# Performance work log

Hardware: AMD Instinct MI355X
Metric: run time of the kernel (lower is better)

The kernel has to match this reference:

```python
import jax, jax.numpy as jnp
import numpy as np

N_HEAD = 16
T0 = 1.0        # eta schedule reference time
C_LOG = 3.0     # fixed eta(t) = C_LOG * log(t / T0)  (mode='log', non-learnable default)
ETA_CLIP = 50.0 # eta clamped to [-ETA_CLIP, ETA_CLIP] before exponentiation


def setup_inputs() -> dict:
    key = jax.random.key(0)
    k0, k1, k2 = jax.random.split(key, 3)
    B, T, D = 2, 2048, 1024
    x = jax.random.normal(k0, (B, T, D), dtype=jnp.float32)
    ln_weight = jnp.ones((D,), dtype=jnp.float32)  # LayerNorm weight (bias=False per cfg)
    c_attn_w = jax.random.normal(k1, (3 * D, D), dtype=jnp.float32) * 0.02  # torch Linear weight [3D, D]
    c_proj_w = jax.random.normal(k2, (D, D), dtype=jnp.float32) * 0.02      # output proj [D, D]
    # theta_h = inv_softplus(1.0) so that step size h = softplus(theta_h) = 1.0
    theta_h = jnp.asarray(np.log(np.expm1(1.0)), dtype=jnp.float32)
    return {"x": x, "ln_weight": ln_weight, "c_attn_w": c_attn_w,
            "c_proj_w": c_proj_w, "theta_h": theta_h}


def _layer_norm(x, w, eps=1e-5):
    mu = jnp.mean(x, axis=-1, keepdims=True)
    var = jnp.var(x, axis=-1, keepdims=True)
    return (x - mu) * jax.lax.rsqrt(var + eps) * w


def reference(x, ln_weight, c_attn_w, c_proj_w, theta_h):
    B, T, D = x.shape
    H = N_HEAD
    hd = D // H

    y = _layer_norm(x, ln_weight)
    qkv = jnp.einsum('btd,ed->bte', y, c_attn_w)        # [B, T, 3D]
    q, k, v = jnp.split(qkv, 3, axis=-1)
    q = q.reshape(B, T, H, hd).transpose(0, 2, 1, 3)    # [B, H, T, hd]
    k = k.reshape(B, T, H, hd).transpose(0, 2, 1, 3)
    v = v.reshape(B, T, H, hd).transpose(0, 2, 1, 3)

    # time-dependent conformal/symplectic scaling: t_i = t0 + h*i, eta = c_log*log(t/t0)
    h = jax.nn.softplus(theta_h)
    t = T0 + h * jnp.arange(T, dtype=jnp.float32)
    eta = jnp.clip(C_LOG * jnp.log(t / T0), -ETA_CLIP, ETA_CLIP)  # [T]
    q = q * jnp.exp(eta)[None, None, :, None]    # query scaled by exp(+eta(t_i))
    k = k * jnp.exp(-eta)[None, None, :, None]   # key scaled by exp(-eta(t_j))

    att = jnp.einsum('bhqd,bhkd->bhqk', q, k) / jnp.sqrt(jnp.float32(hd))
    mask = jnp.tril(jnp.ones((T, T), dtype=bool))  # causal: keep j <= i
    att = jnp.where(mask[None, None], att, -jnp.inf)
    att = jax.nn.softmax(att, axis=-1)

    out = jnp.einsum('bhqk,bhkd->bhqd', att, v)
    out = out.transpose(0, 2, 1, 3).reshape(B, T, D)
    return jnp.einsum('btd,ed->bte', out, c_proj_w)
```

## Files before the change

kernel.cpp:

```cpp
#include <hip/hip_runtime.h>
#include <stdint.h>
#include <stddef.h>

typedef __attribute__((ext_vector_type(8))) short short8;
typedef __attribute__((ext_vector_type(4))) float float4v;

#define T_SEQ 2048
#define D_MODEL 1024
#define NH 16
#define HD 64

static __device__ __forceinline__ unsigned short f2bf(float f) {
  unsigned u = __builtin_bit_cast(unsigned, f);
  u += 0x7fffu + ((u >> 16) & 1u);
  return (unsigned short)(u >> 16);
}
static __device__ __forceinline__ float bf2f(unsigned short h) {
  unsigned u = ((unsigned)h) << 16;
  return __builtin_bit_cast(float, u);
}
static __device__ __forceinline__ float4v mfma16(short8 a, short8 b, float4v c) {
  return __builtin_amdgcn_mfma_f32_16x16x32_bf16(a, b, c, 0, 0, 0);
}
static __device__ __forceinline__ void split3(float f, unsigned short& h0,
                                              unsigned short& h1, unsigned short& h2) {
  h0 = f2bf(f);
  float r1 = f - bf2f(h0);
  h1 = f2bf(r1);
  float r2 = r1 - bf2f(h1);
  h2 = f2bf(r2);
}
static __device__ __forceinline__ void split2(float f, unsigned short& h0, unsigned short& h1) {
  h0 = f2bf(f);
  h1 = f2bf(f - bf2f(h0));
}

static __device__ __forceinline__ void stage16(const unsigned short* g, unsigned short* l) {
#if __has_builtin(__builtin_amdgcn_global_load_lds)
  __builtin_amdgcn_global_load_lds(
      (const __attribute__((address_space(1))) unsigned int*)g,
      (__attribute__((address_space(3))) unsigned int*)l, 16, 0, 0);
#else
  *(short8*)l = *(const short8*)g;
#endif
}

__global__ __launch_bounds__(256) void prep_kernel(
    const float* x, const float* wgt, const float* attn_w, const float* theta,
    unsigned short* y0, unsigned short* y1, unsigned short* y2,
    unsigned short* W0, unsigned short* W1, unsigned short* W2,
    float* E, float* Einv) {
  __shared__ float rs[4], rq[4];
  int bx = blockIdx.x;
  int tid = threadIdx.x;
  if (bx < 4096) {
    int row = bx;
    const float* xr = x + (size_t)row * D_MODEL;
    float v[4];
    float sum = 0.f, ssq = 0.f;
    for (int it = 0; it < 4; ++it) {
      float f = xr[tid + 256 * it];
      v[it] = f;
      sum += f; ssq += f * f;
    }
    for (int off = 32; off >= 1; off >>= 1) {
      sum += __shfl_xor(sum, off, 64);
      ssq += __shfl_xor(ssq, off, 64);
    }
    int w = tid >> 6;
    if ((tid & 63) == 0) { rs[w] = sum; rq[w] = ssq; }
    __syncthreads();
    sum = rs[0] + rs[1] + rs[2] + rs[3];
    ssq = rq[0] + rq[1] + rq[2] + rq[3];
    float mu = sum * (1.0f / D_MODEL);
    float var = ssq * (1.0f / D_MODEL) - mu * mu;
    float rstd = rsqrtf(var + 1e-5f);
    for (int it = 0; it < 4; ++it) {
      int d = tid + 256 * it;
      float y = (v[it] - mu) * rstd * wgt[d];
      unsigned short h0, h1, h2;
      split3(y, h0, h1, h2);
      size_t o = (size_t)row * D_MODEL + d;
      y0[o] = h0; y1[o] = h1; y2[o] = h2;
    }
  } else if (bx < 5632) {
    size_t base = ((size_t)(bx - 4096) * 256 + tid) * 8;
    int row = (int)(base >> 10);
    short8 a, b, c;
    for (int j = 0; j < 8; ++j) {
      unsigned short h0, h1, h2;
      split3(attn_w[base + j], h0, h1, h2);
      a[j] = (short)h0; b[j] = (short)h1; c[j] = (short)h2;
    }
    *(short8*)(W0 + base) = a;
    *(short8*)(W1 + base) = b;
    if (row < 2048) *(short8*)(W2 + base) = c;
  } else {
    int i = (bx - 5632) * 256 + tid;
    if (i < T_SEQ) {
      float th = theta[0];
      float h = log1pf(expf(th));
      float t = 1.0f + h * (float)i;
      float eta = 3.0f * logf(t);
      eta = fminf(fmaxf(eta, -50.0f), 50.0f);
      E[i] = expf(eta);
      Einv[i] = expf(-eta);
    }
  }
}

__global__ __launch_bounds__(256) void conv_pw(const float* src, unsigned short* P0,
                                               unsigned short* P1) {
  size_t base = ((size_t)blockIdx.x * 256 + threadIdx.x) * 8;
  short8 a, b;
  for (int j = 0; j < 8; ++j) {
    unsigned short h0, h1;
    split2(src[base + j], h0, h1);
    a[j] = (short)h0; b[j] = (short)h1;
  }
  *(short8*)(P0 + base) = a;
  *(short8*)(P1 + base) = b;
}


#define RD_A(BUF, MF)                                                           \
  (*(const short8*)(lds_u + (BUF) * 12288 + (wm * 64 + (MF) * 16 + ln) * 32 +   \
                    slot8))
#define RD_B(BUF, NF)                                                           \
  (*(const short8*)(lds_u + (BUF) * 12288 + 8192 +                              \
                    (wn * 64 + (NF) * 16 + ln) * 32 + slot8))

#define STG(BUF, AP, BP, KI)                                                    \
  do {                                                                          \
    const unsigned short* ga = (AP) + (size_t)(m0 + srow) * 1024 + (KI) + kswz8; \
    stage16(ga, lds_u + (BUF) * 12288 + tid * 8);                               \
    stage16(ga + 128 * 1024, lds_u + (BUF) * 12288 + 4096 + tid * 8);           \
    stage16((BP) + (size_t)(brow0 + srow) * 1024 + (KI) + kswz8,                \
            lds_u + (BUF) * 12288 + 8192 + tid * 8);                            \
  } while (0)

#define ASEL(tb) ((tb) == 5 ? y2 : (((tb) & 1) ? y1 : y0))
#define BSEL(tb) (isV ? ((tb) < 2 ? W0 : W1)                                    \
                      : ((tb) < 2 ? W0 : ((tb) < 4 ? W1 : ((tb) == 4 ? W2 : W0))))

#define SBAR __builtin_amdgcn_s_barrier()
#define SCHED0 __builtin_amdgcn_sched_barrier(0)

#define PHASE(BUF, PBUF)                                                        \
  {                                                                             \
    short8 a0 = RD_A(BUF, 0), a1 = RD_A(BUF, 1);                                \
    short8 a2 = RD_A(BUF, 2), a3 = RD_A(BUF, 3);                                \
    short8 b0 = RD_B(BUF, 0), b1 = RD_B(BUF, 1);                                \
    short8 b2 = RD_B(BUF, 2), b3 = RD_B(BUF, 3);                                \
    bool pref = (t + 2 < NKT);                                                  \
    if (pref) {                                                                 \
      int tt = t + 2, tb = tt >> 5, ki = (tt & 31) << 5;                        \
      const unsigned short* Ap = ASEL(tb);                                      \
      const unsigned short* Bp = BSEL(tb);                                      \
      STG(PBUF, Ap, Bp, ki);                                                    \
    }                                                                           \
    SCHED0; SBAR;                                                               \
    asm volatile("s_waitcnt lgkmcnt(0)" ::: "memory");                          \
    SCHED0;                                                                     \
    __builtin_amdgcn_s_setprio(1);                                              \
    acc[0][0] = mfma16(a0, b0, acc[0][0]);                                      \
    acc[0][1] = mfma16(a0, b1, acc[0][1]);                                      \
    acc[0][2] = mfma16(a0, b2, acc[0][2]);                                      \
    acc[0][3] = mfma16(a0, b3, acc[0][3]);                                      \
    acc[1][0] = mfma16(a1, b0, acc[1][0]);                                      \
    acc[1][1] = mfma16(a1, b1, acc[1][1]);                                      \
    acc[1][2] = mfma16(a1, b2, acc[1][2]);                                      \
    acc[1][3] = mfma16(a1, b3, acc[1][3]);                                      \
    acc[2][0] = mfma16(a2, b0, acc[2][0]);                                      \
    acc[2][1] = mfma16(a2, b1, acc[2][1]);                                      \
    acc[2][2] = mfma16(a2, b2, acc[2][2]);                                      \
    acc[2][3] = mfma16(a2, b3, acc[2][3]);                                      \
    acc[3][0] = mfma16(a3, b0, acc[3][0]);                                      \
    acc[3][1] = mfma16(a3, b1, acc[3][1]);                                      \
    acc[3][2] = mfma16(a3, b2, acc[3][2]);                                      \
    acc[3][3] = mfma16(a3, b3, acc[3][3]);                                      \
    __builtin_amdgcn_s_setprio(0);                                              \
    SCHED0;                                                                     \
    if (pref) { asm volatile("s_waitcnt vmcnt(3)" ::: "memory"); }              \
    else      { asm volatile("s_waitcnt vmcnt(0)" ::: "memory"); }              \
    SBAR;                                                                       \
    ++t;                                                                        \
  }

__global__ __launch_bounds__(512, 4) void qkv_ring(
    const unsigned short* __restrict__ y0, const unsigned short* __restrict__ y1,
    const unsigned short* __restrict__ y2, const unsigned short* __restrict__ W0,
    const unsigned short* __restrict__ W1, const unsigned short* __restrict__ W2,
    const float* __restrict__ E, const float* __restrict__ Einv,
    float* __restrict__ Qf, unsigned short* __restrict__ K0,
    unsigned short* __restrict__ K1, unsigned short* __restrict__ K2,
    unsigned short* __restrict__ VbT) {
  extern __shared__ unsigned short lds_u[];
  int tid = threadIdx.x;
  int w = tid >> 6, lane = tid & 63, q4 = lane >> 4, ln = lane & 15;
  int wm = w >> 1, wn = w & 1;
  int slot8 = (q4 ^ ((ln >> 1) & 3)) * 8;
  int srow = tid >> 2;
  int kswz8 = ((tid & 3) ^ ((srow >> 1) & 3)) * 8;

  int bid = blockIdx.x, bx, by;
  if (bid < 256) {
    int wg = ((bid & 7) << 5) | (bid >> 3);
    by = wg >> 4; bx = wg & 15;
  } else {
    int vid = bid - 256;
    int wg = ((vid & 7) << 4) | (vid >> 3);
    by = wg >> 3; bx = 16 + (wg & 7);
  }
  int m0 = by * 256;
  bool isV = (bx >= 16);
  int NKT = isV ? 96 : 192;
  int brow0 = isV ? (2048 + (bx - 16) * 128) : bx * 128;

  float4v zero = {0.f, 0.f, 0.f, 0.f};
  float4v acc[4][4];
#pragma unroll
  for (int mf = 0; mf < 4; ++mf)
#pragma unroll
    for (int nf = 0; nf < 4; ++nf) acc[mf][nf] = zero;

  {
    const unsigned short* Ap = ASEL(0);
    const unsigned short* Bp = BSEL(0);
    STG(0, Ap, Bp, 0);
    STG(1, Ap, Bp, 32);
  }
  asm volatile("s_waitcnt vmcnt(3)" ::: "memory");
  SBAR;

  int t = 0;
  int nit = NKT / 3;
  for (int it = 0; it < nit; ++it) {
    PHASE(0, 2)
    PHASE(1, 0)
    PHASE(2, 1)
  }

  int bi = m0 >> 11, m0g = m0 & 2047;
  if (bx < 8) {
    float* Ql = (float*)lds_u;
    for (int g = 0; g < 2; ++g) {
      if (wn == g) {
#pragma unroll
        for (int mf = 0; mf < 4; ++mf)
#pragma unroll
          for (int nf = 0; nf < 4; ++nf)
#pragma unroll
            for (int r = 0; r < 4; ++r) {
              int rl = wm * 64 + mf * 16 + q4 * 4 + r;
              int tg = m0g + rl;
              Ql[rl * 64 + nf * 16 + ln] = acc[mf][nf][r] * (E[tg] * 0.1803368801f);
            }
      }
      __syncthreads();
      int h = bx * 2 + g;
      float* dst = Qf + ((size_t)(bi * NH + h) * T_SEQ + m0g) * HD;
      for (int itc = 0; itc < 8; ++itc) {
        int idx = itc * 512 + tid;
        *(float4v*)(dst + idx * 4) = *(const float4v*)(Ql + idx * 4);
      }
      __syncthreads();
    }
  } else if (bx < 16) {
    unsigned short* Kl = lds_u;
    for (int g = 0; g < 2; ++g)
      for (int half = 0; half < 2; ++half) {
        if (wn == g && (wm >> 1) == half) {
#pragma unroll
          for (int mf = 0; mf < 4; ++mf)
#pragma unroll
            for (int nf = 0; nf < 4; ++nf)
#pragma unroll
              for (int r = 0; r < 4; ++r) {
                int rlh = (wm & 1) * 64 + mf * 16 + q4 * 4 + r;
                int tg = m0g + half * 128 + rlh;
                unsigned short h0, h1, h2;
                split3(acc[mf][nf][r] * Einv[tg], h0, h1, h2);
                int o = rlh * 64 + nf * 16 + ln;
                Kl[o] = h0; Kl[8192 + o] = h1; Kl[16384 + o] = h2;
              }
        }
        __syncthreads();
        int h = (bx - 8) * 2 + g;
        size_t base = ((size_t)(bi * NH + h) * T_SEQ + m0g + half * 128) * HD;
        for (int itc = 0; itc < 2; ++itc) {
          int idx = itc * 512 + tid;
          *(short8*)(K0 + base + idx * 8) = *(const short8*)(Kl + idx * 8);
          *(short8*)(K1 + base + idx * 8) = *(const short8*)(Kl + 8192 + idx * 8);
          *(short8*)(K2 + base + idx * 8) = *(const short8*)(Kl + 16384 + idx * 8);
        }
        __syncthreads();
      }
  } else {
    unsigned short* Vl = lds_u;
    for (int g = 0; g < 2; ++g) {
      if (wn == g) {
#pragma unroll
        for (int mf = 0; mf < 4; ++mf)
#pragma unroll
          for (int nf = 0; nf < 4; ++nf)
#pragma unroll
            for (int r = 0; r < 4; ++r) {
              int rl = wm * 64 + mf * 16 + q4 * 4 + r;
              int d = nf * 16 + ln;
              Vl[d * 256 + rl] = f2bf(acc[mf][nf][r]);
            }
      }
      __syncthreads();
      int h = (bx - 16) * 2 + g;
      unsigned short* dst = VbT + (size_t)(bi * NH + h) * HD * T_SEQ + m0g;
      for (int itc = 0; itc < 4; ++itc) {
        int idx = itc * 512 + tid;
        int d = idx >> 5, c = idx & 31;
        *(short8*)(dst + (size_t)d * T_SEQ + c * 8) = *(const short8*)(Vl + d * 256 + c * 8);
      }
      __syncthreads();
    }
  }
}
#undef RD_A
#undef RD_B
#undef STG
#undef ASEL
#undef BSEL
#undef PHASE
#undef SBAR
#undef SCHED0

#define ATTN_STAGE(BUF, J0)                                                   \
  for (int i_ = 0; i_ < 2; ++i_) {                                            \
    size_t go_ = (size_t)((J0) + srow + i_ * 32) * 64 + scd * 8;              \
    int lo_ = tid * 8 + i_ * 2048;                                            \
    stage16(Kb0 + go_, &Ks[BUF][0][lo_]);                                     \
    stage16(Kb1 + go_, &Ks[BUF][1][lo_]);                                     \
    stage16(Kb2 + go_, &Ks[BUF][2][lo_]);                                     \
    stage16(Vb + (size_t)(srow + i_ * 32) * T_SEQ + (J0) + scd * 8,           \
            &Vs[BUF][lo_]);                                                   \
  }

#define ATTN_STEP(JT, DIAG)                                                   \
  {                                                                           \
    const int cur_ = (JT) & 1;                                                \
    float p[4][4];                                                            \
    for (int c = 0; c < 4; ++c) {                                             \
      float4v s = zero;                                                       \
      for (int ks = 0; ks < 2; ++ks) {                                        \
        int koff = ((c * 16 + ln) * 8 + ((ks * 4 + q4) ^ swz)) * 8;           \
        short8 k0v = *(const short8*)&Ks[cur_][0][koff];                      \
        short8 k1v = *(const short8*)&Ks[cur_][1][koff];                      \
        short8 k2v = *(const short8*)&Ks[cur_][2][koff];                      \
        s = mfma16(qa[ks][0], k0v, s);                                        \
        s = mfma16(qa[ks][1], k0v, s);                                        \
        s = mfma16(qa[ks][0], k1v, s);                                        \
        s = mfma16(qa[ks][1], k1v, s);                                        \
        s = mfma16(qa[ks][0], k2v, s);                                        \
        s = mfma16(qa[ks][2], k0v, s);                                        \
      }                                                                       \
      if (DIAG) {                                                             \
        int jrow = (JT) * 64 + c * 16 + ln;                                   \
        for (int r = 0; r < 4; ++r)                                           \
          if (jrow > ibase + q4 * 4 + r) s[r] = -3e38f;                       \
      }                                                                       \
      for (int r = 0; r < 4; ++r) p[c][r] = s[r];                             \
    }                                                                         \
    float alpha[4], mnew[4];                                                  \
    for (int r = 0; r < 4; ++r) {                                             \
      float tm = fmaxf(fmaxf(p[0][r], p[1][r]), fmaxf(p[2][r], p[3][r]));     \
      for (int off = 8; off >= 1; off >>= 1)                                  \
        tm = fmaxf(tm, __shfl_xor(tm, off, 16));                              \
      mnew[r] = fmaxf(m_r[r], tm);                                            \
      alpha[r] = exp2f(m_r[r] - mnew[r]);                                     \
      m_r[r] = mnew[r];                                                       \
    }                                                                         \
    for (int c = 0; c < 4; ++c)                                               \
      for (int r = 0; r < 4; ++r) p[c][r] = exp2f(p[c][r] - mnew[r]);         \
    for (int c = 0; c < 4; ++c)                                               \
      for (int r = 0; r < 4; ++r) oacc[c][r] *= alpha[r];                     \
    for (int r = 0; r < 4; ++r) lacc[r] *= alpha[r];                          \
    __asm__ __volatile__("" ::: "memory");                                    \
    for (int c = 0; c < 4; ++c)                                               \
      for (int r = 0; r < 4; ++r)                                             \
        Plds[w][q4 * 4 + r][c * 16 + ln] =                                    \
            (unsigned short)(__builtin_bit_cast(unsigned, p[c][r]) >> 16);    \
    __asm__ __volatile__("" ::: "memory");                                    \
    for (int ks = 0; ks < 2; ++ks) {                                          \
      short8 pa = *(const short8*)&Plds[w][ln][ks * 32 + q4 * 8];             \
      for (int c = 0; c < 4; ++c) {                                           \
        int voff = ((c * 16 + ln) * 8 + ((ks * 4 + q4) ^ swz)) * 8;           \
        short8 vb = *(const short8*)&Vs[cur_][voff];                          \
        oacc[c] = mfma16(pa, vb, oacc[c]);                                    \
      }                                                                       \
      lacc = mfma16(pa, ones, lacc);                                          \
    }                                                                         \
    __asm__ __volatile__("" ::: "memory");                                    \
  }

__global__ __launch_bounds__(256) void attn_kernel(
    const float* Qf, const unsigned short* K0, const unsigned short* K1,
    const unsigned short* K2, const unsigned short* VbT,
    unsigned short* Ob0, unsigned short* Ob1) {
  __shared__ unsigned short Ks[2][3][4096];
  __shared__ unsigned short Vs[2][4096];
  __shared__ unsigned short Plds[4][16][72];
  int tid = threadIdx.x;
  int w = tid >> 6, lane = tid & 63, q4 = lane >> 4, ln = lane & 15;
  int bidx = blockIdx.x;
  int bh = ((bidx & 7) << 2) | ((bidx >> 3) & 3);
  int px = bidx >> 5;
  const float* Qb = Qf + (size_t)bh * T_SEQ * HD;
  const unsigned short* Kb0 = K0 + (size_t)bh * T_SEQ * HD;
  const unsigned short* Kb1 = K1 + (size_t)bh * T_SEQ * HD;
  const unsigned short* Kb2 = K2 + (size_t)bh * T_SEQ * HD;
  const unsigned short* Vb = VbT + (size_t)bh * HD * T_SEQ;
  int b = bh >> 4, hh = bh & 15;
  float4v zero = {0.f, 0.f, 0.f, 0.f};
  short8 ones;
  for (int j = 0; j < 8; ++j) ones[j] = (short)(unsigned short)0x3F80;

  int srow = tid >> 3, scs = tid & 7;
  int scd = scs ^ (srow & 7);
  int swz = ln & 7;

  for (int half = 0; half < 2; ++half) {
    int qt = half ? (31 - px) : px;
    int q0 = qt * 64;
    int ibase = q0 + w * 16;

    short8 qa[2][3];
    {
      const float* qp = Qb + (size_t)(ibase + ln) * HD;
      for (int ks = 0; ks < 2; ++ks) {
        float f[8];
        *(float4v*)&f[0] = *(const float4v*)(qp + ks * 32 + q4 * 8);
        *(float4v*)&f[4] = *(const float4v*)(qp + ks * 32 + q4 * 8 + 4);
        for (int j = 0; j < 8; ++j) {
          unsigned short h0, h1, h2;
          split3(f[j], h0, h1, h2);
          qa[ks][0][j] = (short)h0; qa[ks][1][j] = (short)h1; qa[ks][2][j] = (short)h2;
        }
      }
    }

    float m_r[4] = {-3e38f, -3e38f, -3e38f, -3e38f};
    float4v lacc = zero;
    float4v oacc[4];
    for (int c = 0; c < 4; ++c) oacc[c] = zero;

    __syncthreads();
    ATTN_STAGE(0, 0)
    for (int jt = 0; jt < qt; ++jt) {
      __syncthreads();
      ATTN_STAGE((jt + 1) & 1, (jt + 1) * 64)
      ATTN_STEP(jt, 0)
    }
    __syncthreads();
    ATTN_STEP(qt, 1)

    for (int c = 0; c < 4; ++c)
      for (int r = 0; r < 4; ++r) {
        int i = ibase + q4 * 4 + r;
        float val = oacc[c][r] / lacc[r];
        unsigned short h0, h1;
        split2(val, h0, h1);
        size_t o = ((size_t)(b * T_SEQ + i)) * D_MODEL + hh * 64 + c * 16 + ln;
        Ob0[o] = h0; Ob1[o] = h1;
      }
  }
}
#undef ATTN_STAGE
#undef ATTN_STEP

__global__ __launch_bounds__(256) void proj_gemm(
    const unsigned short* A0, const unsigned short* A1,
    const unsigned short* P0, const unsigned short* P1, float* out) {
  __shared__ unsigned short SB[4 * 4096];
  int tid = threadIdx.x;
  int w = tid >> 6, lane = tid & 63, q4 = lane >> 4, ln = lane & 15;
  int wr = w >> 1, wc = w & 1;
  int n0g = blockIdx.x * 128;
  int m0 = blockIdx.y * 128;
  const unsigned short* Asrc[2] = {A0, A1};
  const unsigned short* Bsrc[2] = {P0, P1};

  float4v zero = {0.f, 0.f, 0.f, 0.f};
  float4v acc[4][4];
  for (int mt = 0; mt < 4; ++mt)
    for (int ct = 0; ct < 4; ++ct) acc[mt][ct] = zero;

  int srow = tid >> 2, kpart = tid & 3;
  int kswz = kpart ^ ((srow >> 1) & 3);
  int slot8 = (q4 ^ ((ln >> 1) & 3)) * 8;
  unsigned lds_off = (unsigned)tid * 16;

  for (int k0 = 0; k0 < D_MODEL; k0 += 32) {
    __syncthreads();
    for (int i = 0; i < 2; ++i) {
      size_t arow = (size_t)(m0 + srow + i * 64) * D_MODEL + k0 + kswz * 8;
      size_t brow = (size_t)(n0g + srow + i * 64) * D_MODEL + k0 + kswz * 8;
      for (int s = 0; s < 2; ++s) {
        stage16(Asrc[s] + arow, (unsigned short*)((char*)(SB + s * 4096) + lds_off + i * 4096));
        stage16(Bsrc[s] + brow, (unsigned short*)((char*)(SB + (2 + s) * 4096) + lds_off + i * 4096));
      }
    }
    __syncthreads();

    short8 af[4][2];
    for (int mt = 0; mt < 4; ++mt)
      for (int s = 0; s < 2; ++s)
        af[mt][s] = *(const short8*)(SB + s * 4096 + (wr * 64 + mt * 16 + ln) * 32 + slot8);
    for (int ct = 0; ct < 4; ++ct) {
      int brow = (wc * 64 + ct * 16 + ln) * 32 + slot8;
      short8 b0 = *(const short8*)(SB + 2 * 4096 + brow);
      short8 b1 = *(const short8*)(SB + 3 * 4096 + brow);
      for (int mt = 0; mt < 4; ++mt) {
        float4v a = acc[mt][ct];
        a = mfma16(af[mt][0], b0, a);
        a = mfma16(af[mt][1], b0, a);
        a = mfma16(af[mt][0], b1, a);
        acc[mt][ct] = a;
      }
    }
  }

  for (int mt = 0; mt < 4; ++mt)
    for (int ct = 0; ct < 4; ++ct)
      for (int r = 0; r < 4; ++r) {
        int gm = m0 + wr * 64 + mt * 16 + q4 * 4 + r;
        int col = n0g + wc * 64 + ct * 16 + ln;
        out[(size_t)gm * D_MODEL + col] = acc[mt][ct][r];
      }
}

extern "C" void kernel_launch(void* const* d_in, const int* in_sizes, int n_in,
                              void* d_out, int out_size, void* d_ws, size_t ws_size,
                              hipStream_t stream) {
  const float* x      = (const float*)d_in[0];
  const float* ln_w   = (const float*)d_in[1];
  const float* attn_w = (const float*)d_in[2];
  const float* proj_w = (const float*)d_in[3];
  const float* theta  = (const float*)d_in[4];
  float* out = (float*)d_out;

  char* ws = (char*)d_ws;
  const size_t SZY  = (size_t)4096 * 1024 * 2;
  const size_t SZW  = (size_t)3072 * 1024 * 2;
  const size_t SZW2 = (size_t)2048 * 1024 * 2;
  const size_t SZQ  = (size_t)2 * 16 * 2048 * 64 * 4;
  const size_t SZK  = (size_t)2 * 16 * 2048 * 64 * 2;

  unsigned short* y0 = (unsigned short*)(ws);
  unsigned short* y1 = (unsigned short*)(ws + SZY);
  unsigned short* y2 = (unsigned short*)(ws + 2 * SZY);
  unsigned short* W0 = (unsigned short*)(ws + 3 * SZY);
  unsigned short* W1 = (unsigned short*)(ws + 3 * SZY + SZW);
  unsigned short* W2 = (unsigned short*)(ws + 3 * SZY + 2 * SZW);
  float* Qf          = (float*)(ws + 3 * SZY + 2 * SZW + SZW2);
  unsigned short* K0 = (unsigned short*)(ws + 3 * SZY + 2 * SZW + SZW2 + SZQ);
  unsigned short* K1 = (unsigned short*)(ws + 3 * SZY + 2 * SZW + SZW2 + SZQ + SZK);
  float* E           = (float*)(ws + 3 * SZY + 2 * SZW + SZW2 + SZQ + 2 * SZK);
  float* Einv        = E + T_SEQ;
  unsigned short* Ob0 = y0;
  unsigned short* Ob1 = y1;
  unsigned short* PW0 = y2;
  unsigned short* PW1 = y2 + (size_t)1024 * 1024;
  unsigned short* VbT = (unsigned short*)d_out;
  unsigned short* K2  = (unsigned short*)((char*)d_out + SZK);

  size_t needed = 3 * SZY + 2 * SZW + SZW2 + SZQ + 2 * SZK + 2 * T_SEQ * 4;
  if (ws_size < needed) return;

  static int lds_cfg = 0;
  if (!lds_cfg) {
    hipFuncSetAttribute((const void*)qkv_ring,
                        hipFuncAttributeMaxDynamicSharedMemorySize, 73728);
    lds_cfg = 1;
  }

  prep_kernel<<<dim3(5640), dim3(256), 0, stream>>>(x, ln_w, attn_w, theta,
                                                    y0, y1, y2, W0, W1, W2, E, Einv);
  qkv_ring<<<dim3(384), dim3(512), 73728, stream>>>(y0, y1, y2, W0, W1, W2, E, Einv,
                                                    Qf, K0, K1, K2, VbT);
  conv_pw<<<dim3(512), dim3(256), 0, stream>>>(proj_w, PW0, PW1);
  attn_kernel<<<dim3(512), dim3(256), 0, stream>>>(Qf, K0, K1, K2, VbT, Ob0, Ob1);
  proj_gemm<<<dim3(8, 32), dim3(256), 0, stream>>>(Ob0, Ob1, PW0, PW1, out);
}
```

Baseline: 377.7 us.

## Process 128-row query tiles per block with two M-fragments per wave

Measured after the change: 408.4 us. +8.1%, slower.

```diff
diff --git a/kernel.cpp b/kernel.cpp
--- a/kernel.cpp
+++ b/kernel.cpp
@@ -346,58 +346,74 @@
 #define ATTN_STEP(JT, DIAG)                                                   \
   {                                                                           \
     const int cur_ = (JT) & 1;                                                \
-    float p[4][4];                                                            \
+    float p[2][4][4];                                                         \
     for (int c = 0; c < 4; ++c) {                                             \
-      float4v s = zero;                                                       \
+      float4v s0 = zero, s1 = zero;                                           \
       for (int ks = 0; ks < 2; ++ks) {                                        \
         int koff = ((c * 16 + ln) * 8 + ((ks * 4 + q4) ^ swz)) * 8;           \
         short8 k0v = *(const short8*)&Ks[cur_][0][koff];                      \
         short8 k1v = *(const short8*)&Ks[cur_][1][koff];                      \
         short8 k2v = *(const short8*)&Ks[cur_][2][koff];                      \
-        s = mfma16(qa[ks][0], k0v, s);                                        \
-        s = mfma16(qa[ks][1], k0v, s);                                        \
-        s = mfma16(qa[ks][0], k1v, s);                                        \
-        s = mfma16(qa[ks][1], k1v, s);                                        \
-        s = mfma16(qa[ks][0], k2v, s);                                        \
-        s = mfma16(qa[ks][2], k0v, s);                                        \
+        s0 = mfma16(qa[0][ks][0], k0v, s0);                                   \
+        s0 = mfma16(qa[0][ks][1], k0v, s0);                                   \
+        s0 = mfma16(qa[0][ks][0], k1v, s0);                                   \
+        s0 = mfma16(qa[0][ks][1], k1v, s0);                                   \
+        s0 = mfma16(qa[0][ks][0], k2v, s0);                                   \
+        s0 = mfma16(qa[0][ks][2], k0v, s0);                                   \
+        s1 = mfma16(qa[1][ks][0], k0v, s1);                                   \
+        s1 = mfma16(qa[1][ks][1], k0v, s1);                                   \
+        s1 = mfma16(qa[1][ks][0], k1v, s1);                                   \
+        s1 = mfma16(qa[1][ks][1], k1v, s1);                                   \
+        s1 = mfma16(qa[1][ks][0], k2v, s1);                                   \
+        s1 = mfma16(qa[1][ks][2], k0v, s1);                                   \
       }                                                                       \
       if (DIAG) {                                                             \
         int jrow = (JT) * 64 + c * 16 + ln;                                   \
+        for (int r = 0; r < 4; ++r) {                                         \
+          if (jrow > ibase + q4 * 4 + r) s0[r] = -3e38f;                      \
+          if (jrow > ibase + 16 + q4 * 4 + r) s1[r] = -3e38f;                 \
+        }                                                                     \
+      }                                                                       \
+      for (int r = 0; r < 4; ++r) { p[0][c][r] = s0[r]; p[1][c][r] = s1[r]; } \
+    }                                                                         \
+    float alpha[2][4];                                                        \
+    for (int mf = 0; mf < 2; ++mf)                                            \
+      for (int r = 0; r < 4; ++r) {                                           \
+        float tm = fmaxf(fmaxf(p[mf][0][r], p[mf][1][r]),                     \
+                         fmaxf(p[mf][2][r], p[mf][3][r]));                    \
+        for (int off = 8; off >= 1; off >>= 1)                                \
+          tm = fmaxf(tm, __shfl_xor(tm, off, 16));                            \
+        float mnew = fmaxf(m_r[mf][r], tm);                                   \
+        alpha[mf][r] = exp2f(m_r[mf][r] - mnew);                              \
+        m_r[mf][r] = mnew;                                                    \
+      }                                                                       \
+    for (int mf = 0; mf < 2; ++mf)                                            \
+      for (int c = 0; c < 4; ++c)                                             \
         for (int r = 0; r < 4; ++r)                                           \
-          if (jrow > ibase + q4 * 4 + r) s[r] = -3e38f;                       \
+          p[mf][c][r] = exp2f(p[mf][c][r] - m_r[mf][r]);                      \
+    for (int mf = 0; mf < 2; ++mf) {                                          \
+      for (int c = 0; c < 4; ++c)                                             \
+        for (int r = 0; r < 4; ++r) oacc[mf][c][r] *= alpha[mf][r];           \
+      for (int r = 0; r < 4; ++r) lacc[mf][r] *= alpha[mf][r];                \
+    }                                                                         \
+    for (int mf = 0; mf < 2; ++mf) {                                          \
+      __asm__ __volatile__("" ::: "memory");                                  \
+      for (int c = 0; c < 4; ++c)                                             \
+        for (int r = 0; r < 4; ++r)                                           \
+          Plds[w][q4 * 4 + r][c * 16 + ln] =                                  \
+              (unsigned short)(__builtin_bit_cast(unsigned, p[mf][c][r]) >> 16); \
+      __asm__ __volatile__("" ::: "memory");                                  \
+      for (int ks = 0; ks < 2; ++ks) {                                        \
+        short8 pa = *(const short8*)&Plds[w][ln][ks * 32 + q4 * 8];           \
+        for (int c = 0; c < 4; ++c) {                                         \
+          int voff = ((c * 16 + ln) * 8 + ((ks * 4 + q4) ^ swz)) * 8;         \
+          short8 vb = *(const short8*)&Vs[cur_][voff];                        \
+          oacc[mf][c] = mfma16(pa, vb, oacc[mf][c]);                          \
+        }                                                                     \
+        lacc[mf] = mfma16(pa, ones, lacc[mf]);                                \
       }                                                                       \
-      for (int r = 0; r < 4; ++r) p[c][r] = s[r];                             \
+      __asm__ __volatile__("" ::: "memory");                                  \
     }                                                                         \
-    float alpha[4], mnew[4];                                                  \
-    for (int r = 0; r < 4; ++r) {                                             \
-      float tm = fmaxf(fmaxf(p[0][r], p[1][r]), fmaxf(p[2][r], p[3][r]));     \
-      for (int off = 8; off >= 1; off >>= 1)                                  \
-        tm = fmaxf(tm, __shfl_xor(tm, off, 16));                              \
-      mnew[r] = fmaxf(m_r[r], tm);                                            \
-      alpha[r] = exp2f(m_r[r] - mnew[r]);                                     \
-      m_r[r] = mnew[r];                                                       \
-    }                                                                         \
-    for (int c = 0; c < 4; ++c)                                               \
-      for (int r = 0; r < 4; ++r) p[c][r] = exp2f(p[c][r] - mnew[r]);         \
-    for (int c = 0; c < 4; ++c)                                               \
-      for (int r = 0; r < 4; ++r) oacc[c][r] *= alpha[r];                     \
-    for (int r = 0; r < 4; ++r) lacc[r] *= alpha[r];                          \
-    __asm__ __volatile__("" ::: "memory");                                    \
-    for (int c = 0; c < 4; ++c)                                               \
-      for (int r = 0; r < 4; ++r)                                             \
-        Plds[w][q4 * 4 + r][c * 16 + ln] =                                    \
-            (unsigned short)(__builtin_bit_cast(unsigned, p[c][r]) >> 16);    \
-    __asm__ __volatile__("" ::: "memory");                                    \
-    for (int ks = 0; ks < 2; ++ks) {                                          \
-      short8 pa = *(const short8*)&Plds[w][ln][ks * 32 + q4 * 8];             \
-      for (int c = 0; c < 4; ++c) {                                           \
-        int voff = ((c * 16 + ln) * 8 + ((ks * 4 + q4) ^ swz)) * 8;           \
-        short8 vb = *(const short8*)&Vs[cur_][voff];                          \
-        oacc[c] = mfma16(pa, vb, oacc[c]);                                    \
-      }                                                                       \
-      lacc = mfma16(pa, ones, lacc);                                          \
-    }                                                                         \
-    __asm__ __volatile__("" ::: "memory");                                    \
   }
 
 __global__ __launch_bounds__(256) void attn_kernel(
@@ -411,7 +427,8 @@
   int w = tid >> 6, lane = tid & 63, q4 = lane >> 4, ln = lane & 15;
   int bidx = blockIdx.x;
   int bh = ((bidx & 7) << 2) | ((bidx >> 3) & 3);
-  int px = bidx >> 5;
+  int u = bidx >> 5;
+  int tl = (u < 8) ? u : (23 - u);
   const float* Qb = Qf + (size_t)bh * T_SEQ * HD;
   const unsigned short* Kb0 = K0 + (size_t)bh * T_SEQ * HD;
   const unsigned short* Kb1 = K1 + (size_t)bh * T_SEQ * HD;
@@ -426,51 +443,55 @@
   int scd = scs ^ (srow & 7);
   int swz = ln & 7;
 
-  for (int half = 0; half < 2; ++half) {
-    int qt = half ? (31 - px) : px;
-    int q0 = qt * 64;
-    int ibase = q0 + w * 16;
-
-    short8 qa[2][3];
-    {
-      const float* qp = Qb + (size_t)(ibase + ln) * HD;
-      for (int ks = 0; ks < 2; ++ks) {
-        float f[8];
-        *(float4v*)&f[0] = *(const float4v*)(qp + ks * 32 + q4 * 8);
-        *(float4v*)&f[4] = *(const float4v*)(qp + ks * 32 + q4 * 8 + 4);
-        for (int j = 0; j < 8; ++j) {
-          unsigned short h0, h1, h2;
-          split3(f[j], h0, h1, h2);
-          qa[ks][0][j] = (short)h0; qa[ks][1][j] = (short)h1; qa[ks][2][j] = (short)h2;
-        }
-      }
-    }
-
-    float m_r[4] = {-3e38f, -3e38f, -3e38f, -3e38f};
-    float4v lacc = zero;
-    float4v oacc[4];
-    for (int c = 0; c < 4; ++c) oacc[c] = zero;
-
+  int ibase = tl * 128 + w * 32;
+  int NT = 2 * tl + 2;
+
+  short8 qa[2][2][3];
+  for (int mf = 0; mf < 2; ++mf) {
+    const float* qp = Qb + (size_t)(ibase + mf * 16 + ln) * HD;
+    for (int ks = 0; ks < 2; ++ks) {
+      float f[8];
+      *(float4v*)&f[0] = *(const float4v*)(qp + ks * 32 + q4 * 8);
+      *(float4v*)&f[4] = *(const float4v*)(qp + ks * 32 + q4 * 8 + 4);
+      for (int j = 0; j < 8; ++j) {
+        unsigned short h0, h1, h2;
+        split3(f[j], h0, h1, h2);
+        qa[mf][ks][0][j] = (short)h0; qa[mf][ks][1][j] = (short)h1;
+        qa[mf][ks][2][j] = (short)h2;
+      }
+    }
+  }
+
+  float m_r[2][4];
+  for (int mf = 0; mf < 2; ++mf)
+    for (int r = 0; r < 4; ++r) m_r[mf][r] = -3e38f;
+  float4v lacc[2] = {zero, zero};
+  float4v oacc[2][4];
+  for (int mf = 0; mf < 2; ++mf)
+    for (int c = 0; c < 4; ++c) oacc[mf][c] = zero;
+
+  ATTN_STAGE(0, 0)
+  for (int jt = 0; jt < NT - 2; ++jt) {
     __syncthreads();
-    ATTN_STAGE(0, 0)
-    for (int jt = 0; jt < qt; ++jt) {
-      __syncthreads();
-      ATTN_STAGE((jt + 1) & 1, (jt + 1) * 64)
-      ATTN_STEP(jt, 0)
-    }
-    __syncthreads();
-    ATTN_STEP(qt, 1)
-
+    ATTN_STAGE((jt + 1) & 1, (jt + 1) * 64)
+    ATTN_STEP(jt, 0)
+  }
+  __syncthreads();
+  ATTN_STAGE((NT - 1) & 1, (NT - 1) * 64)
+  ATTN_STEP(NT - 2, 1)
+  __syncthreads();
+  ATTN_STEP(NT - 1, 1)
+
+  for (int mf = 0; mf < 2; ++mf)
     for (int c = 0; c < 4; ++c)
       for (int r = 0; r < 4; ++r) {
-        int i = ibase + q4 * 4 + r;
-        float val = oacc[c][r] / lacc[r];
+        int i = ibase + mf * 16 + q4 * 4 + r;
+        float val = oacc[mf][c][r] / lacc[mf][r];
         unsigned short h0, h1;
         split2(val, h0, h1);
         size_t o = ((size_t)(b * T_SEQ + i)) * D_MODEL + hh * 64 + c * 16 + ln;
         Ob0[o] = h0; Ob1[o] = h1;
       }
-  }
 }
 #undef ATTN_STAGE
 #undef ATTN_STEP
```
